# Optimization experiments

Hardware: AMD Instinct MI355X
Metric: run time of the kernel (lower is better)

The kernel has to match this reference:

```python
import jax, jax.numpy as jnp
import numpy as np

N = 1_000_000
D = 64      # input_size
O = 64      # output_size


def setup_inputs() -> dict:
    key = jax.random.key(0)
    k1, k2, k3, k4, k5 = jax.random.split(key, 5)
    x = jax.random.normal(k1, (N, D), dtype=jnp.float32)
    item_to_left_idxs = jax.random.randint(k2, (N,), 0, N, dtype=jnp.int64 if jax.config.jax_enable_x64 else jnp.int32)
    item_to_right_idxs = jax.random.randint(k3, (N,), 0, N, dtype=jnp.int64 if jax.config.jax_enable_x64 else jnp.int32)
    # nn.Linear(3*D, O): weight [O, 3*D], bias [O]
    bound = 1.0 / np.sqrt(3 * D)
    W = jax.random.uniform(k4, (O, 3 * D), dtype=jnp.float32, minval=-bound, maxval=bound)
    b = jax.random.uniform(k5, (O,), dtype=jnp.float32, minval=-bound, maxval=bound)
    return {"x": x, "item_to_left_idxs": item_to_left_idxs,
            "item_to_right_idxs": item_to_right_idxs, "W": W, "b": b}


def reference(x, item_to_left_idxs, item_to_right_idxs, W, b):
    # cat((x, x[left], x[right]), -1) @ W.T + b
    # Expressed as three smaller GEMMs on the weight slices to avoid
    # materializing the [N, 3D] concat (same math as the torch module).
    Wx, Wl, Wr = W[:, :D], W[:, D:2 * D], W[:, 2 * D:]
    out = (jnp.einsum('nd,od->no', x, Wx)
           + jnp.einsum('nd,od->no', x[item_to_left_idxs], Wl)
           + jnp.einsum('nd,od->no', x[item_to_right_idxs], Wr)
           + b)
    return out
```

## Files before the change

kernel.cpp:

```cpp
#include <hip/hip_runtime.h>


typedef __bf16 bf16x8 __attribute__((ext_vector_type(8)));
typedef float floatx4 __attribute__((ext_vector_type(4)));

#define D 64
#define O 64
#define K3 192

__global__ __launch_bounds__(256) void convert_x_bf16(
    const float* __restrict__ x, __bf16* __restrict__ xb, long n8)
{
    long i = (long)blockIdx.x * 256 + threadIdx.x;
    const long stride = (long)gridDim.x * 256;
    for (; i < n8; i += stride) {
        floatx4 a = __builtin_nontemporal_load((const floatx4*)x + 2 * i);
        floatx4 b = __builtin_nontemporal_load((const floatx4*)x + 2 * i + 1);
        bf16x8 f;
        f[0] = (__bf16)a[0]; f[1] = (__bf16)a[1];
        f[2] = (__bf16)a[2]; f[3] = (__bf16)a[3];
        f[4] = (__bf16)b[0]; f[5] = (__bf16)b[1];
        f[6] = (__bf16)b[2]; f[7] = (__bf16)b[3];
        ((bf16x8*)xb)[i] = f;
    }
}

__device__ __forceinline__ void issue_gather_bf16(bf16x8 (&v)[6],
                                                  const __bf16* __restrict__ xb,
                                                  int item, int li, int ri, int quad) {
    const __bf16* px = xb + (size_t)item * D + quad * 8;
    const __bf16* pl = xb + (size_t)li   * D + quad * 8;
    const __bf16* pr = xb + (size_t)ri   * D + quad * 8;
    v[0] = *(const bf16x8*)(px); v[1] = *(const bf16x8*)(px + 32);
    v[2] = *(const bf16x8*)(pl); v[3] = *(const bf16x8*)(pl + 32);
    v[4] = *(const bf16x8*)(pr); v[5] = *(const bf16x8*)(pr + 32);
}

__device__ __forceinline__ void compute_store_bf16(const bf16x8 (&v)[6],
                                                   const bf16x8 (&bfrag)[6][4],
                                                   const float (&bi)[4],
                                                   float* __restrict__ out,
                                                   int base, int col, int quad) {
    floatx4 acc[4];
#pragma unroll
    for (int ct = 0; ct < 4; ++ct)
        acc[ct] = (floatx4){bi[ct], bi[ct], bi[ct], bi[ct]};
#pragma unroll
    for (int ct = 0; ct < 4; ++ct)
#pragma unroll
        for (int ks = 0; ks < 6; ++ks)
            acc[ct] = __builtin_amdgcn_mfma_f32_16x16x32_bf16(
                v[ks], bfrag[ks][ct], acc[ct], 0, 0, 0);

    float* orow = out + (size_t)base * O;
#pragma unroll
    for (int ct = 0; ct < 4; ++ct)
#pragma unroll
        for (int r = 0; r < 4; ++r) {
            int m = quad * 4 + r;
            __builtin_nontemporal_store(acc[ct][r],
                                        orow + (size_t)m * O + ct * 16 + col);
        }
}

__global__ __launch_bounds__(256, 2) void polyconv_bf16(
    const __bf16* __restrict__ xb,
    const int* __restrict__ lidx,
    const int* __restrict__ ridx,
    const float* __restrict__ W,
    const float* __restrict__ bias,
    float* __restrict__ out,
    int n_tiles, int total_waves)
{
    const int lane = threadIdx.x & 63;
    const int wave_id = blockIdx.x * (blockDim.x >> 6) + (threadIdx.x >> 6);
    const int col  = lane & 15;
    const int quad = lane >> 4;

    bf16x8 bfrag[6][4];
#pragma unroll
    for (int ct = 0; ct < 4; ++ct) {
        const float* wrow = W + (size_t)(ct * 16 + col) * K3 + quad * 8;
#pragma unroll
        for (int ks = 0; ks < 6; ++ks) {
            floatx4 w0 = *(const floatx4*)(wrow + ks * 32);
            floatx4 w1 = *(const floatx4*)(wrow + ks * 32 + 4);
            bf16x8 f;
            f[0] = (__bf16)w0[0]; f[1] = (__bf16)w0[1];
            f[2] = (__bf16)w0[2]; f[3] = (__bf16)w0[3];
            f[4] = (__bf16)w1[0]; f[5] = (__bf16)w1[1];
            f[6] = (__bf16)w1[2]; f[7] = (__bf16)w1[3];
            bfrag[ks][ct] = f;
        }
    }
    float bi[4];
#pragma unroll
    for (int ct = 0; ct < 4; ++ct) bi[ct] = bias[ct * 16 + col];

    const int stride = total_waves;
    int t = wave_id;
    if (t >= n_tiles) return;

    bf16x8 va[6], vb[6];
    int li_n = 0, ri_n = 0;

    {
        int item = t * 16 + col;
        int li = lidx[item], ri = ridx[item];
        issue_gather_bf16(va, xb, item, li, ri, quad);
    }
    int t1 = t + stride;
    if (t1 < n_tiles) { li_n = lidx[t1 * 16 + col]; ri_n = ridx[t1 * 16 + col]; }

    while (true) {
        if (t1 < n_tiles) {
            issue_gather_bf16(vb, xb, t1 * 16 + col, li_n, ri_n, quad);
            int t2 = t1 + stride;
            if (t2 < n_tiles) { li_n = lidx[t2 * 16 + col]; ri_n = ridx[t2 * 16 + col]; }
        }
        compute_store_bf16(va, bfrag, bi, out, t * 16, col, quad);
        t = t1; t1 += stride;
        if (t >= n_tiles) break;

        if (t1 < n_tiles) {
            issue_gather_bf16(va, xb, t1 * 16 + col, li_n, ri_n, quad);
            int t2 = t1 + stride;
            if (t2 < n_tiles) { li_n = lidx[t2 * 16 + col]; ri_n = ridx[t2 * 16 + col]; }
        }
        compute_store_bf16(vb, bfrag, bi, out, t * 16, col, quad);
        t = t1; t1 += stride;
        if (t >= n_tiles) break;
    }
}

__device__ __forceinline__ void issue_gather_f32(floatx4 (&v)[12], const float* __restrict__ x,
                                                 int item, int li, int ri, int quad) {
    const float* px = x + (size_t)item * D + quad * 8;
    const float* pl = x + (size_t)li   * D + quad * 8;
    const float* pr = x + (size_t)ri   * D + quad * 8;
    v[0]  = *(const floatx4*)(px);      v[1]  = *(const floatx4*)(px + 4);
    v[2]  = *(const floatx4*)(px + 32); v[3]  = *(const floatx4*)(px + 36);
    v[4]  = *(const floatx4*)(pl);      v[5]  = *(const floatx4*)(pl + 4);
    v[6]  = *(const floatx4*)(pl + 32); v[7]  = *(const floatx4*)(pl + 36);
    v[8]  = *(const floatx4*)(pr);      v[9]  = *(const floatx4*)(pr + 4);
    v[10] = *(const floatx4*)(pr + 32); v[11] = *(const floatx4*)(pr + 36);
}

__device__ __forceinline__ void compute_store_f32(const floatx4 (&v)[12],
                                                  const bf16x8 (&bfrag)[6][4],
                                                  const float (&bi)[4],
                                                  float* __restrict__ out,
                                                  int base, int col, int quad) {
    bf16x8 afrag[6];
#pragma unroll
    for (int ks = 0; ks < 6; ++ks) {
        floatx4 a0 = v[2 * ks], a1 = v[2 * ks + 1];
        bf16x8 f;
        f[0] = (__bf16)a0[0]; f[1] = (__bf16)a0[1];
        f[2] = (__bf16)a0[2]; f[3] = (__bf16)a0[3];
        f[4] = (__bf16)a1[0]; f[5] = (__bf16)a1[1];
        f[6] = (__bf16)a1[2]; f[7] = (__bf16)a1[3];
        afrag[ks] = f;
    }
    floatx4 acc[4];
#pragma unroll
    for (int ct = 0; ct < 4; ++ct)
        acc[ct] = (floatx4){bi[ct], bi[ct], bi[ct], bi[ct]};
#pragma unroll
    for (int ct = 0; ct < 4; ++ct)
#pragma unroll
        for (int ks = 0; ks < 6; ++ks)
            acc[ct] = __builtin_amdgcn_mfma_f32_16x16x32_bf16(
                afrag[ks], bfrag[ks][ct], acc[ct], 0, 0, 0);

    float* orow = out + (size_t)base * O;
#pragma unroll
    for (int ct = 0; ct < 4; ++ct)
#pragma unroll
        for (int r = 0; r < 4; ++r) {
            int m = quad * 4 + r;
            __builtin_nontemporal_store(acc[ct][r],
                                        orow + (size_t)m * O + ct * 16 + col);
        }
}

__global__ __launch_bounds__(256, 2) void polyconv_kernel(
    const float* __restrict__ x,
    const int* __restrict__ lidx,
    const int* __restrict__ ridx,
    const float* __restrict__ W,
    const float* __restrict__ bias,
    float* __restrict__ out,
    int n_tiles, int total_waves)
{
    const int lane = threadIdx.x & 63;
    const int wave_id = blockIdx.x * (blockDim.x >> 6) + (threadIdx.x >> 6);
    const int col  = lane & 15;
    const int quad = lane >> 4;

    bf16x8 bfrag[6][4];
#pragma unroll
    for (int ct = 0; ct < 4; ++ct) {
        const float* wrow = W + (size_t)(ct * 16 + col) * K3 + quad * 8;
#pragma unroll
        for (int ks = 0; ks < 6; ++ks) {
            floatx4 w0 = *(const floatx4*)(wrow + ks * 32);
            floatx4 w1 = *(const floatx4*)(wrow + ks * 32 + 4);
            bf16x8 f;
            f[0] = (__bf16)w0[0]; f[1] = (__bf16)w0[1];
            f[2] = (__bf16)w0[2]; f[3] = (__bf16)w0[3];
            f[4] = (__bf16)w1[0]; f[5] = (__bf16)w1[1];
            f[6] = (__bf16)w1[2]; f[7] = (__bf16)w1[3];
            bfrag[ks][ct] = f;
        }
    }
    float bi[4];
#pragma unroll
    for (int ct = 0; ct < 4; ++ct) bi[ct] = bias[ct * 16 + col];

    const int stride = total_waves;
    int t = wave_id;
    if (t >= n_tiles) return;

    floatx4 va[12], vb[12];
    int li_n = 0, ri_n = 0;

    {
        int item = t * 16 + col;
        int li = lidx[item], ri = ridx[item];
        issue_gather_f32(va, x, item, li, ri, quad);
    }
    int t1 = t + stride;
    if (t1 < n_tiles) { li_n = lidx[t1 * 16 + col]; ri_n = ridx[t1 * 16 + col]; }

    while (true) {
        if (t1 < n_tiles) {
            issue_gather_f32(vb, x, t1 * 16 + col, li_n, ri_n, quad);
            int t2 = t1 + stride;
            if (t2 < n_tiles) { li_n = lidx[t2 * 16 + col]; ri_n = ridx[t2 * 16 + col]; }
        }
        compute_store_f32(va, bfrag, bi, out, t * 16, col, quad);
        t = t1; t1 += stride;
        if (t >= n_tiles) break;

        if (t1 < n_tiles) {
            issue_gather_f32(va, x, t1 * 16 + col, li_n, ri_n, quad);
            int t2 = t1 + stride;
            if (t2 < n_tiles) { li_n = lidx[t2 * 16 + col]; ri_n = ridx[t2 * 16 + col]; }
        }
        compute_store_f32(vb, bfrag, bi, out, t * 16, col, quad);
        t = t1; t1 += stride;
        if (t >= n_tiles) break;
    }
}

extern "C" void kernel_launch(void* const* d_in, const int* in_sizes, int n_in,
                              void* d_out, int out_size, void* d_ws, size_t ws_size,
                              hipStream_t stream) {
    const float* x  = (const float*)d_in[0];
    const int*   li = (const int*)d_in[1];
    const int*   ri = (const int*)d_in[2];
    const float* W  = (const float*)d_in[3];
    const float* b  = (const float*)d_in[4];
    float* out = (float*)d_out;

    const int n = in_sizes[1];
    const int n_tiles = n / 16;
    const size_t need = (size_t)n * D * sizeof(__bf16);

    if (d_ws != nullptr && ws_size >= need) {
        __bf16* xb = (__bf16*)d_ws;
        const long n8 = (long)n * D / 8;
        convert_x_bf16<<<2048, 256, 0, stream>>>(x, xb, n8);

        const int blocks = 1024;
        const int total_waves = blocks * 4;
        polyconv_bf16<<<blocks, 256, 0, stream>>>(xb, li, ri, W, b, out,
                                                  n_tiles, total_waves);
    } else {
        const int blocks = 1024;
        const int total_waves = blocks * 4;
        polyconv_kernel<<<blocks, 256, 0, stream>>>(x, li, ri, W, b, out,
                                                    n_tiles, total_waves);
    }
}
```

Baseline: 537.8 us.

## Fuse bf16 conversion into gather-GEMM via cooperative grid sync; swap MFMA operands for vector stores

The fp32-to-bf16 conversion and the gather-GEMM kernel are merged into one cooperative kernel that converts x, loads the weight fragments, then grid-syncs before the gather loop. This removes the second launch and the inter-kernel gap, and lets each wave load weights while other blocks are still converting. The MFMA operands are also swapped so each lane holds four consecutive output columns, which allows 16-byte vector nontemporal stores instead of scalar ones, and the bias is loaded as float4. The cost is a grid-wide barrier and a grid sized by occupancy (up to 1024 blocks on 256 CUs), with a fallback to the old two-kernel path if the cooperative launch fails.

```diff
diff --git a/kernel.cpp b/kernel.cpp
--- a/kernel.cpp
+++ b/kernel.cpp
@@ -1,4 +1,7 @@
 #include <hip/hip_runtime.h>
+#include <hip/hip_cooperative_groups.h>
+
+namespace cg = cooperative_groups;
 
 
 typedef __bf16 bf16x8 __attribute__((ext_vector_type(8)));
@@ -8,20 +11,37 @@
 #define O 64
 #define K3 192
 
-__global__ __launch_bounds__(256) void convert_x_bf16(
-    const float* __restrict__ x, __bf16* __restrict__ xb, long n8)
-{
-    long i = (long)blockIdx.x * 256 + threadIdx.x;
-    const long stride = (long)gridDim.x * 256;
-    for (; i < n8; i += stride) {
-        floatx4 a = __builtin_nontemporal_load((const floatx4*)x + 2 * i);
-        floatx4 b = __builtin_nontemporal_load((const floatx4*)x + 2 * i + 1);
-        bf16x8 f;
-        f[0] = (__bf16)a[0]; f[1] = (__bf16)a[1];
-        f[2] = (__bf16)a[2]; f[3] = (__bf16)a[3];
-        f[4] = (__bf16)b[0]; f[5] = (__bf16)b[1];
-        f[6] = (__bf16)b[2]; f[7] = (__bf16)b[3];
-        ((bf16x8*)xb)[i] = f;
+__device__ __forceinline__ void cvt_chunk(const float* __restrict__ x,
+                                          __bf16* __restrict__ xb, long i) {
+    floatx4 a = __builtin_nontemporal_load((const floatx4*)x + 2 * i);
+    floatx4 b = __builtin_nontemporal_load((const floatx4*)x + 2 * i + 1);
+    bf16x8 f;
+    f[0] = (__bf16)a[0]; f[1] = (__bf16)a[1];
+    f[2] = (__bf16)a[2]; f[3] = (__bf16)a[3];
+    f[4] = (__bf16)b[0]; f[5] = (__bf16)b[1];
+    f[6] = (__bf16)b[2]; f[7] = (__bf16)b[3];
+    ((bf16x8*)xb)[i] = f;
+}
+
+__device__ __forceinline__ void load_wfrags(bf16x8 (&bfrag)[6][4], floatx4 (&bi4)[4],
+                                            const float* __restrict__ W,
+                                            const float* __restrict__ bias,
+                                            int col, int quad) {
+#pragma unroll
+    for (int ct = 0; ct < 4; ++ct) {
+        const float* wrow = W + (size_t)(ct * 16 + col) * K3 + quad * 8;
+#pragma unroll
+        for (int ks = 0; ks < 6; ++ks) {
+            floatx4 w0 = *(const floatx4*)(wrow + ks * 32);
+            floatx4 w1 = *(const floatx4*)(wrow + ks * 32 + 4);
+            bf16x8 f;
+            f[0] = (__bf16)w0[0]; f[1] = (__bf16)w0[1];
+            f[2] = (__bf16)w0[2]; f[3] = (__bf16)w0[3];
+            f[4] = (__bf16)w1[0]; f[5] = (__bf16)w1[1];
+            f[6] = (__bf16)w1[2]; f[7] = (__bf16)w1[3];
+            bfrag[ks][ct] = f;
+        }
+        bi4[ct] = *(const floatx4*)(bias + ct * 16 + quad * 4);
     }
 }
 
@@ -36,31 +56,107 @@
     v[4] = *(const bf16x8*)(pr); v[5] = *(const bf16x8*)(pr + 32);
 }
 
-__device__ __forceinline__ void compute_store_bf16(const bf16x8 (&v)[6],
-                                                   const bf16x8 (&bfrag)[6][4],
-                                                   const float (&bi)[4],
-                                                   float* __restrict__ out,
-                                                   int base, int col, int quad) {
+__device__ __forceinline__ void compute_store_swapped(const bf16x8 (&v)[6],
+                                                      const bf16x8 (&bfrag)[6][4],
+                                                      const floatx4 (&bi4)[4],
+                                                      float* __restrict__ out,
+                                                      int base, int col, int quad) {
     floatx4 acc[4];
 #pragma unroll
-    for (int ct = 0; ct < 4; ++ct)
-        acc[ct] = (floatx4){bi[ct], bi[ct], bi[ct], bi[ct]};
+    for (int ct = 0; ct < 4; ++ct) acc[ct] = bi4[ct];
 #pragma unroll
     for (int ct = 0; ct < 4; ++ct)
 #pragma unroll
         for (int ks = 0; ks < 6; ++ks)
             acc[ct] = __builtin_amdgcn_mfma_f32_16x16x32_bf16(
-                v[ks], bfrag[ks][ct], acc[ct], 0, 0, 0);
-
-    float* orow = out + (size_t)base * O;
+                bfrag[ks][ct], v[ks], acc[ct], 0, 0, 0);
+    float* op = out + (size_t)(base + col) * O + quad * 4;
 #pragma unroll
     for (int ct = 0; ct < 4; ++ct)
-#pragma unroll
-        for (int r = 0; r < 4; ++r) {
-            int m = quad * 4 + r;
-            __builtin_nontemporal_store(acc[ct][r],
-                                        orow + (size_t)m * O + ct * 16 + col);
-        }
+        __builtin_nontemporal_store(acc[ct], (floatx4*)(op + ct * 16));
+}
+
+__device__ __forceinline__ void gather_compute_loop(const __bf16* __restrict__ xb,
+                                                    const int* __restrict__ lidx,
+                                                    const int* __restrict__ ridx,
+                                                    const bf16x8 (&bfrag)[6][4],
+                                                    const floatx4 (&bi4)[4],
+                                                    float* __restrict__ out,
+                                                    int n_tiles, int stride,
+                                                    int wave_id, int col, int quad) {
+    int t = wave_id;
+    if (t >= n_tiles) return;
+
+    bf16x8 va[6], vb[6];
+    int li_n = 0, ri_n = 0;
+
+    {
+        int item = t * 16 + col;
+        int li = lidx[item], ri = ridx[item];
+        issue_gather_bf16(va, xb, item, li, ri, quad);
+    }
+    int t1 = t + stride;
+    if (t1 < n_tiles) { li_n = lidx[t1 * 16 + col]; ri_n = ridx[t1 * 16 + col]; }
+
+    while (true) {
+        if (t1 < n_tiles) {
+            issue_gather_bf16(vb, xb, t1 * 16 + col, li_n, ri_n, quad);
+            int t2 = t1 + stride;
+            if (t2 < n_tiles) { li_n = lidx[t2 * 16 + col]; ri_n = ridx[t2 * 16 + col]; }
+        }
+        compute_store_swapped(va, bfrag, bi4, out, t * 16, col, quad);
+        t = t1; t1 += stride;
+        if (t >= n_tiles) break;
+
+        if (t1 < n_tiles) {
+            issue_gather_bf16(va, xb, t1 * 16 + col, li_n, ri_n, quad);
+            int t2 = t1 + stride;
+            if (t2 < n_tiles) { li_n = lidx[t2 * 16 + col]; ri_n = ridx[t2 * 16 + col]; }
+        }
+        compute_store_swapped(vb, bfrag, bi4, out, t * 16, col, quad);
+        t = t1; t1 += stride;
+        if (t >= n_tiles) break;
+    }
+}
+
+__global__ __launch_bounds__(256, 2) void polyconv_fused(
+    const float* __restrict__ x,
+    const int* __restrict__ lidx,
+    const int* __restrict__ ridx,
+    const float* __restrict__ W,
+    const float* __restrict__ bias,
+    float* __restrict__ out,
+    __bf16* __restrict__ xb,
+    int n_tiles, int total_waves, long n8)
+{
+    const int lane = threadIdx.x & 63;
+    const int wave_id = blockIdx.x * (blockDim.x >> 6) + (threadIdx.x >> 6);
+    const int col  = lane & 15;
+    const int quad = lane >> 4;
+
+    {
+        long i = (long)blockIdx.x * blockDim.x + threadIdx.x;
+        const long cstride = (long)gridDim.x * blockDim.x;
+        for (; i < n8; i += cstride) cvt_chunk(x, xb, i);
+    }
+
+    bf16x8 bfrag[6][4];
+    floatx4 bi4[4];
+    load_wfrags(bfrag, bi4, W, bias, col, quad);
+
+    __threadfence();
+    cg::this_grid().sync();
+
+    gather_compute_loop(xb, lidx, ridx, bfrag, bi4, out,
+                        n_tiles, total_waves, wave_id, col, quad);
+}
+
+__global__ __launch_bounds__(256) void convert_x_bf16(
+    const float* __restrict__ x, __bf16* __restrict__ xb, long n8)
+{
+    long i = (long)blockIdx.x * 256 + threadIdx.x;
+    const long stride = (long)gridDim.x * 256;
+    for (; i < n8; i += stride) cvt_chunk(x, xb, i);
 }
 
 __global__ __launch_bounds__(256, 2) void polyconv_bf16(
@@ -78,59 +174,11 @@
     const int quad = lane >> 4;
 
     bf16x8 bfrag[6][4];
-#pragma unroll
-    for (int ct = 0; ct < 4; ++ct) {
-        const float* wrow = W + (size_t)(ct * 16 + col) * K3 + quad * 8;
-#pragma unroll
-        for (int ks = 0; ks < 6; ++ks) {
-            floatx4 w0 = *(const floatx4*)(wrow + ks * 32);
-            floatx4 w1 = *(const floatx4*)(wrow + ks * 32 + 4);
-            bf16x8 f;
-            f[0] = (__bf16)w0[0]; f[1] = (__bf16)w0[1];
-            f[2] = (__bf16)w0[2]; f[3] = (__bf16)w0[3];
-            f[4] = (__bf16)w1[0]; f[5] = (__bf16)w1[1];
-            f[6] = (__bf16)w1[2]; f[7] = (__bf16)w1[3];
-            bfrag[ks][ct] = f;
-        }
-    }
-    float bi[4];
-#pragma unroll
-    for (int ct = 0; ct < 4; ++ct) bi[ct] = bias[ct * 16 + col];
-
-    const int stride = total_waves;
-    int t = wave_id;
-    if (t >= n_tiles) return;
-
-    bf16x8 va[6], vb[6];
-    int li_n = 0, ri_n = 0;
-
-    {
-        int item = t * 16 + col;
-        int li = lidx[item], ri = ridx[item];
-        issue_gather_bf16(va, xb, item, li, ri, quad);
-    }
-    int t1 = t + stride;
-    if (t1 < n_tiles) { li_n = lidx[t1 * 16 + col]; ri_n = ridx[t1 * 16 + col]; }
-
-    while (true) {
-        if (t1 < n_tiles) {
-            issue_gather_bf16(vb, xb, t1 * 16 + col, li_n, ri_n, quad);
-            int t2 = t1 + stride;
-            if (t2 < n_tiles) { li_n = lidx[t2 * 16 + col]; ri_n = ridx[t2 * 16 + col]; }
-        }
-        compute_store_bf16(va, bfrag, bi, out, t * 16, col, quad);
-        t = t1; t1 += stride;
-        if (t >= n_tiles) break;
-
-        if (t1 < n_tiles) {
-            issue_gather_bf16(va, xb, t1 * 16 + col, li_n, ri_n, quad);
-            int t2 = t1 + stride;
-            if (t2 < n_tiles) { li_n = lidx[t2 * 16 + col]; ri_n = ridx[t2 * 16 + col]; }
-        }
-        compute_store_bf16(vb, bfrag, bi, out, t * 16, col, quad);
-        t = t1; t1 += stride;
-        if (t >= n_tiles) break;
-    }
+    floatx4 bi4[4];
+    load_wfrags(bfrag, bi4, W, bias, col, quad);
+
+    gather_compute_loop(xb, lidx, ridx, bfrag, bi4, out,
+                        n_tiles, total_waves, wave_id, col, quad);
 }
 
 __device__ __forceinline__ void issue_gather_f32(floatx4 (&v)[12], const float* __restrict__ x,
@@ -144,44 +192,6 @@
     v[6]  = *(const floatx4*)(pl + 32); v[7]  = *(const floatx4*)(pl + 36);
     v[8]  = *(const floatx4*)(pr);      v[9]  = *(const floatx4*)(pr + 4);
     v[10] = *(const floatx4*)(pr + 32); v[11] = *(const floatx4*)(pr + 36);
-}
-
-__device__ __forceinline__ void compute_store_f32(const floatx4 (&v)[12],
-                                                  const bf16x8 (&bfrag)[6][4],
-                                                  const float (&bi)[4],
-                                                  float* __restrict__ out,
-                                                  int base, int col, int quad) {
-    bf16x8 afrag[6];
-#pragma unroll
-    for (int ks = 0; ks < 6; ++ks) {
-        floatx4 a0 = v[2 * ks], a1 = v[2 * ks + 1];
-        bf16x8 f;
-        f[0] = (__bf16)a0[0]; f[1] = (__bf16)a0[1];
-        f[2] = (__bf16)a0[2]; f[3] = (__bf16)a0[3];
-        f[4] = (__bf16)a1[0]; f[5] = (__bf16)a1[1];
-        f[6] = (__bf16)a1[2]; f[7] = (__bf16)a1[3];
-        afrag[ks] = f;
-    }
-    floatx4 acc[4];
-#pragma unroll
-    for (int ct = 0; ct < 4; ++ct)
-        acc[ct] = (floatx4){bi[ct], bi[ct], bi[ct], bi[ct]};
-#pragma unroll
-    for (int ct = 0; ct < 4; ++ct)
-#pragma unroll
-        for (int ks = 0; ks < 6; ++ks)
-            acc[ct] = __builtin_amdgcn_mfma_f32_16x16x32_bf16(
-                afrag[ks], bfrag[ks][ct], acc[ct], 0, 0, 0);
-
-    float* orow = out + (size_t)base * O;
-#pragma unroll
-    for (int ct = 0; ct < 4; ++ct)
-#pragma unroll
-        for (int r = 0; r < 4; ++r) {
-            int m = quad * 4 + r;
-            __builtin_nontemporal_store(acc[ct][r],
-                                        orow + (size_t)m * O + ct * 16 + col);
-        }
 }
 
 __global__ __launch_bounds__(256, 2) void polyconv_kernel(
@@ -199,24 +209,8 @@
     const int quad = lane >> 4;
 
     bf16x8 bfrag[6][4];
-#pragma unroll
-    for (int ct = 0; ct < 4; ++ct) {
-        const float* wrow = W + (size_t)(ct * 16 + col) * K3 + quad * 8;
-#pragma unroll
-        for (int ks = 0; ks < 6; ++ks) {
-            floatx4 w0 = *(const floatx4*)(wrow + ks * 32);
-            floatx4 w1 = *(const floatx4*)(wrow + ks * 32 + 4);
-            bf16x8 f;
-            f[0] = (__bf16)w0[0]; f[1] = (__bf16)w0[1];
-            f[2] = (__bf16)w0[2]; f[3] = (__bf16)w0[3];
-            f[4] = (__bf16)w1[0]; f[5] = (__bf16)w1[1];
-            f[6] = (__bf16)w1[2]; f[7] = (__bf16)w1[3];
-            bfrag[ks][ct] = f;
-        }
-    }
-    float bi[4];
-#pragma unroll
-    for (int ct = 0; ct < 4; ++ct) bi[ct] = bias[ct * 16 + col];
+    floatx4 bi4[4];
+    load_wfrags(bfrag, bi4, W, bias, col, quad);
 
     const int stride = total_waves;
     int t = wave_id;
@@ -239,7 +233,20 @@
             int t2 = t1 + stride;
             if (t2 < n_tiles) { li_n = lidx[t2 * 16 + col]; ri_n = ridx[t2 * 16 + col]; }
         }
-        compute_store_f32(va, bfrag, bi, out, t * 16, col, quad);
+        {
+            bf16x8 af[6];
+#pragma unroll
+            for (int ks = 0; ks < 6; ++ks) {
+                floatx4 a0 = va[2 * ks], a1 = va[2 * ks + 1];
+                bf16x8 f;
+                f[0] = (__bf16)a0[0]; f[1] = (__bf16)a0[1];
+                f[2] = (__bf16)a0[2]; f[3] = (__bf16)a0[3];
+                f[4] = (__bf16)a1[0]; f[5] = (__bf16)a1[1];
+                f[6] = (__bf16)a1[2]; f[7] = (__bf16)a1[3];
+                af[ks] = f;
+            }
+            compute_store_swapped(af, bfrag, bi4, out, t * 16, col, quad);
+        }
         t = t1; t1 += stride;
         if (t >= n_tiles) break;
 
@@ -248,7 +255,20 @@
             int t2 = t1 + stride;
             if (t2 < n_tiles) { li_n = lidx[t2 * 16 + col]; ri_n = ridx[t2 * 16 + col]; }
         }
-        compute_store_f32(vb, bfrag, bi, out, t * 16, col, quad);
+        {
+            bf16x8 af[6];
+#pragma unroll
+            for (int ks = 0; ks < 6; ++ks) {
+                floatx4 a0 = vb[2 * ks], a1 = vb[2 * ks + 1];
+                bf16x8 f;
+                f[0] = (__bf16)a0[0]; f[1] = (__bf16)a0[1];
+                f[2] = (__bf16)a0[2]; f[3] = (__bf16)a0[3];
+                f[4] = (__bf16)a1[0]; f[5] = (__bf16)a1[1];
+                f[6] = (__bf16)a1[2]; f[7] = (__bf16)a1[3];
+                af[ks] = f;
+            }
+            compute_store_swapped(af, bfrag, bi4, out, t * 16, col, quad);
+        }
         t = t1; t1 += stride;
         if (t >= n_tiles) break;
     }
@@ -267,20 +287,38 @@
     const int n = in_sizes[1];
     const int n_tiles = n / 16;
     const size_t need = (size_t)n * D * sizeof(__bf16);
+    const long n8 = (long)n * D / 8;
 
     if (d_ws != nullptr && ws_size >= need) {
         __bf16* xb = (__bf16*)d_ws;
-        const long n8 = (long)n * D / 8;
+
+        static int coop_blocks = -1;
+        if (coop_blocks < 0) {
+            int maxb = 0;
+            if (hipOccupancyMaxActiveBlocksPerMultiprocessor(
+                    &maxb, polyconv_fused, 256, 0) != hipSuccess || maxb < 1)
+                maxb = 2;
+            if (maxb > 4) maxb = 4;
+            coop_blocks = 256 * maxb;
+        }
+
+        int blocks = coop_blocks;
+        int total_waves = blocks * 4;
+        void* args[] = {(void*)&x, (void*)&li, (void*)&ri, (void*)&W, (void*)&b,
+                        (void*)&out, (void*)&xb, (void*)&n_tiles,
+                        (void*)&total_waves, (void*)&n8};
+        hipError_t e = hipLaunchCooperativeKernel(
+            (const void*)polyconv_fused, dim3(blocks), dim3(256), args, 0, stream);
+        if (e == hipSuccess) return;
+
+        (void)hipGetLastError();
         convert_x_bf16<<<2048, 256, 0, stream>>>(x, xb, n8);
-
-        const int blocks = 1024;
-        const int total_waves = blocks * 4;
-        polyconv_bf16<<<blocks, 256, 0, stream>>>(xb, li, ri, W, b, out,
-                                                  n_tiles, total_waves);
+        const int blocks2 = 1024;
+        polyconv_bf16<<<blocks2, 256, 0, stream>>>(xb, li, ri, W, b, out,
+                                                   n_tiles, blocks2 * 4);
     } else {
         const int blocks = 1024;
-        const int total_waves = blocks * 4;
         polyconv_kernel<<<blocks, 256, 0, stream>>>(x, li, ri, W, b, out,
-                                                    n_tiles, total_waves);
-    }
-}
+                                                    n_tiles, blocks * 4);
+    }
+}
```

Measured after the change: 597.5 us. +11.1%, slower.
